# Kernel optimization log

Hardware: AMD Instinct MI355X
Metric: run time of the kernel (lower is better)

The kernel has to match this reference:

```python
import jax, jax.numpy as jnp
import numpy as np

DN = ('NHWC', 'HWIO', 'NHWC')

def _conv1x1(x, k):
    # 1x1 conv, stride 1, SAME padding (channels_last)
    return jax.lax.conv_general_dilated(x, k, window_strides=(1, 1), padding='SAME', dimension_numbers=DN)

def setup_inputs() -> dict:
    key = jax.random.key(0)
    k1, k2, k3, k4, k5 = jax.random.split(key, 5)
    B, H, W, C = 4, 64, 64, 256
    c8 = C // 8
    x = jax.random.normal(k1, (B, H, W, C), dtype=jnp.float32)
    # Glorot-like scaling for stability
    kernel_f = jax.random.normal(k2, (1, 1, C, c8), dtype=jnp.float32) * (1.0 / np.sqrt(C))
    kernel_g = jax.random.normal(k3, (1, 1, C, c8), dtype=jnp.float32) * (1.0 / np.sqrt(C))
    kernel_h = jax.random.normal(k4, (1, 1, C, C), dtype=jnp.float32) * (1.0 / np.sqrt(C))
    gamma = jax.random.normal(k5, (), dtype=jnp.float32) * 0.1
    return {'x': x, 'kernel_f': kernel_f, 'kernel_g': kernel_g, 'kernel_h': kernel_h, 'gamma': gamma}

def reference(x, kernel_f, kernel_g, kernel_h, gamma):
    B, H, W, C = x.shape
    N = H * W
    f = _conv1x1(x, kernel_f).reshape(B, N, -1)   # [B, N, C/8] queries
    g = _conv1x1(x, kernel_g).reshape(B, N, -1)   # [B, N, C/8] keys
    h = _conv1x1(x, kernel_h).reshape(B, N, -1)   # [B, N, C]   values
    e = jnp.einsum('bnc,bmc->bnm', f, g)          # [B, N, N] scores
    attn = jax.nn.softmax(e, axis=-1)
    o = jnp.einsum('bnm,bmc->bnc', attn, h).reshape(B, H, W, C)
    return x + gamma * o
```

## Files before the change

kernel.cpp:

```cpp
#include <hip/hip_runtime.h>

typedef __attribute__((ext_vector_type(8))) short bf16x8;
typedef __attribute__((ext_vector_type(4))) float f32x4;
typedef __attribute__((ext_vector_type(16))) float f32x16;

__device__ __forceinline__ unsigned short f2bf(float f) {
    union { float f; unsigned u; } v; v.f = f;
    return (unsigned short)((v.u + 0x7FFFu + ((v.u >> 16) & 1u)) >> 16);
}
__device__ __forceinline__ unsigned f2bf2_fast(float a, float b) {
    union { float f; unsigned u; } va, vb; va.f = a; vb.f = b;
    return ((va.u + 0x8000u) >> 16) | ((vb.u + 0x8000u) & 0xFFFF0000u);
}

__device__ __forceinline__ void async16(unsigned short* lds, const unsigned short* gsrc) {
    __builtin_amdgcn_global_load_lds(
        (const __attribute__((address_space(1))) void*)gsrc,
        (__attribute__((address_space(3))) void*)lds, 16, 0, 0);
}

__global__ __launch_bounds__(256) void k_wt(const float* __restrict__ kf,
                                            const float* __restrict__ kg,
                                            const float* __restrict__ kh,
                                            unsigned short* __restrict__ wt) {
    int n = blockIdx.x, t = threadIdx.x;
    const float* src; int stride, col;
    if (n < 32)      { src = kf; stride = 32;  col = n; }
    else if (n < 64) { src = kg; stride = 32;  col = n - 32; }
    else             { src = kh; stride = 256; col = n - 64; }
    wt[n * 256 + (((t >> 3) ^ (n & 7)) << 3) + (t & 7)] = f2bf(src[t * stride + col]);
}

__global__ __launch_bounds__(512) void k_proj(const float* __restrict__ x,
                                              const unsigned short* __restrict__ wt,
                                              unsigned short* __restrict__ f,
                                              unsigned short* __restrict__ g,
                                              unsigned short* __restrict__ hT) {
    __shared__ unsigned short xs[16384];
    __shared__ unsigned short ws[2][16384];
    int t = threadIdx.x, rb = blockIdx.x;
    int w = t >> 6, lane = t & 63, q = lane >> 4, n15 = lane & 15;
    int b = rb >> 6, nbase = (rb & 63) * 64;

#pragma unroll
    for (int i = 0; i < 8; ++i) {
        int lin = i * 512 + t, row = lin >> 6, c4 = lin & 63;
        float4 v = *(const float4*)&x[(rb * 64 + row) * 256 + c4 * 4];
        ushort4 o; o.x = f2bf(v.x); o.y = f2bf(v.y); o.z = f2bf(v.z); o.w = f2bf(v.w);
        *(ushort4*)&xs[row * 256 + (((c4 >> 1) ^ (row & 7)) << 3) + ((c4 & 1) << 2)] = o;
    }
#pragma unroll
    for (int j = 0; j < 4; ++j)
        async16(&ws[0][(j * 512 + w * 64) * 8], wt + (j * 512 + t) * 8);

    for (int ct = 0; ct < 5; ++ct) {
        int cur = ct & 1, nxt = cur ^ 1;
        __syncthreads();
        if (ct < 4) {
            const unsigned short* wsrc = wt + (ct + 1) * 16384;
#pragma unroll
            for (int j = 0; j < 4; ++j)
                async16(&ws[nxt][(j * 512 + w * 64) * 8], wsrc + (j * 512 + t) * 8);
        }
        const unsigned short* wcur = ws[cur];
        f32x4 acc[2];
        acc[0] = (f32x4){0.f, 0.f, 0.f, 0.f};
        acc[1] = (f32x4){0.f, 0.f, 0.f, 0.f};

        if (ct == 0) {
            int rg = w & 3, cg = w >> 2;
#pragma unroll
            for (int kk = 0; kk < 8; ++kk) {
                bf16x8 a = *(const bf16x8*)&xs[(rg * 16 + n15) * 256
                                + ((((kk << 2) + q) ^ (n15 & 7)) << 3)];
#pragma unroll
                for (int nt = 0; nt < 2; ++nt) {
                    bf16x8 bw = *(const bf16x8*)&wcur[(cg * 32 + nt * 16 + n15) * 256
                                    + ((((kk << 2) + q) ^ (n15 & 7)) << 3)];
                    acc[nt] = __builtin_amdgcn_mfma_f32_16x16x32_bf16(a, bw, acc[nt], 0, 0, 0);
                }
            }
#pragma unroll
            for (int nt = 0; nt < 2; ++nt)
#pragma unroll
                for (int r = 0; r < 4; ++r) {
                    int grow = rb * 64 + rg * 16 + q * 4 + r;
                    int col = cg * 32 + nt * 16 + n15;
                    unsigned short v = f2bf(acc[nt][r]);
                    if (col < 32) f[grow * 32 + col] = v;
                    else          g[grow * 32 + (col - 32)] = v;
                }
        } else {
            int cg = w & 3, rg = w >> 2;
#pragma unroll
            for (int kk = 0; kk < 8; ++kk) {
                bf16x8 a = *(const bf16x8*)&wcur[(cg * 16 + n15) * 256
                                + ((((kk << 2) + q) ^ (n15 & 7)) << 3)];
#pragma unroll
                for (int nt = 0; nt < 2; ++nt) {
                    bf16x8 bx = *(const bf16x8*)&xs[(rg * 32 + nt * 16 + n15) * 256
                                    + ((((kk << 2) + q) ^ (n15 & 7)) << 3)];
                    acc[nt] = __builtin_amdgcn_mfma_f32_16x16x32_bf16(a, bx, acc[nt], 0, 0, 0);
                }
            }
#pragma unroll
            for (int nt = 0; nt < 2; ++nt)
#pragma unroll
                for (int r = 0; r < 4; ++r) {
                    int ch = (ct - 1) * 64 + cg * 16 + q * 4 + r;
                    int nloc = nbase + rg * 32 + nt * 16 + n15;
                    hT[b * 1048576 + ch * 4096 + nloc] = f2bf(acc[nt][r]);
                }
        }
    }
}

__global__ __launch_bounds__(512, 4) void k_attn(const float* __restrict__ x,
                                                 const unsigned short* __restrict__ f,
                                                 const unsigned short* __restrict__ g,
                                                 const unsigned short* __restrict__ hT,
                                                 const float* __restrict__ gamma_p,
                                                 float* __restrict__ out) {
    __shared__ unsigned short hs[2][8192];
    __shared__ unsigned short pls[2][4096];
    __shared__ float lrec[64];
    int t = threadIdx.x, bx = blockIdx.x;
    int b = (bx >> 1) & 3;
    int ch2 = (bx >> 3) & 1;
    int qt = ((bx & 1) << 5) | (bx >> 4);
    int qbase = qt * 64;
    int chbase = ch2 * 128;
    int w = t >> 6, l = t & 63;
    int hi = l >> 5, l31 = l & 31;
    int q = l >> 4, n15 = l & 15;
    int cb = w & 3;
    const bool is_s = (w < 4);

    bf16x8 aFB;
    if (is_s)
        aFB = *(const bf16x8*)&f[(b * 4096 + qbase + w * 16 + n15) * 32 + q * 8];

    const unsigned short* hsrc = hT + b * 1048576 + (chbase + (t >> 3)) * 4096
                               + (((t & 7) ^ ((t >> 3) & 7)) << 3);

    const unsigned short* gbase = g + (b * 4096 + n15) * 32 + q * 8;
    bf16x8 aG[4], aGn[4];

    f32x16 o0, o1;
#pragma unroll
    for (int i = 0; i < 16; ++i) { o0[i] = 0.f; o1[i] = 0.f; }
    float l_acc = 0.f;
    const f32x4 zero4 = (f32x4){0.f, 0.f, 0.f, 0.f};

    auto s_tile = [&](int buf) {
        f32x4 sa[4];
#pragma unroll
        for (int nt = 0; nt < 4; ++nt)
            sa[nt] = __builtin_amdgcn_mfma_f32_16x16x32_bf16(aG[nt], aFB, zero4, 0, 0, 0);
#pragma unroll
        for (int nt = 0; nt < 4; ++nt)
#pragma unroll
            for (int r = 0; r < 4; ++r) {
                sa[nt][r] = __expf(sa[nt][r]);
                l_acc += sa[nt][r];
            }
#pragma unroll
        for (int nt = 0; nt < 4; ++nt) {
            unsigned p0 = f2bf2_fast(sa[nt][0], sa[nt][1]);
            unsigned p1 = f2bf2_fast(sa[nt][2], sa[nt][3]);
            int kq = 4 * nt + q;
            unsigned* dst = (unsigned*)&pls[buf][(w * 16 + n15) * 64]
                          + ((kq >> 1) ^ (n15 & 7)) * 4 + (kq & 1) * 2;
            dst[0] = p0; dst[1] = p1;
        }
    };

    async16(&hs[0][w * 512], hsrc);
    async16(&hs[0][4096 + w * 512], hsrc + 64 * 4096);
    if (is_s) {
#pragma unroll
        for (int nt = 0; nt < 4; ++nt)
            aG[nt] = *(const bf16x8*)&gbase[(nt * 16) * 32];
#pragma unroll
        for (int nt = 0; nt < 4; ++nt)
            aGn[nt] = *(const bf16x8*)&gbase[(64 + nt * 16) * 32];
        s_tile(0);
#pragma unroll
        for (int nt = 0; nt < 4; ++nt) aG[nt] = aGn[nt];
    }
    __syncthreads();

    for (int kt = 0; kt < 64; ++kt) {
        int cur = kt & 1, nxt = cur ^ 1;

        if (kt + 1 < 64) {
            const unsigned short* hp = hsrc + (kt + 1) * 64;
            async16(&hs[nxt][w * 512], hp);
            async16(&hs[nxt][4096 + w * 512], hp + 64 * 4096);
        }

        if (is_s) {
            if (kt + 1 < 64) {
                int ktn = (kt + 2 < 64) ? kt + 2 : 63;
#pragma unroll
                for (int nt = 0; nt < 4; ++nt)
                    aGn[nt] = *(const bf16x8*)&gbase[(ktn * 64 + nt * 16) * 32];
                s_tile(nxt);
#pragma unroll
                for (int nt = 0; nt < 4; ++nt) aG[nt] = aGn[nt];
            }
        } else {
            const unsigned short* hcur = &hs[cur][0];
            const unsigned short* pcur = &pls[cur][0];
#pragma unroll
            for (int ks = 0; ks < 4; ++ks) {
                int seg = (((2 * ks + hi) ^ (l31 & 7)) << 3);
                bf16x8 bH  = *(const bf16x8*)&hcur[(cb * 32 + l31) * 64 + seg];
                bf16x8 aP0 = *(const bf16x8*)&pcur[l31 * 64 + seg];
                bf16x8 aP1 = *(const bf16x8*)&pcur[(32 + l31) * 64 + seg];
                o0 = __builtin_amdgcn_mfma_f32_32x32x16_bf16(aP0, bH, o0, 0, 0, 0);
                o1 = __builtin_amdgcn_mfma_f32_32x32x16_bf16(aP1, bH, o1, 0, 0, 0);
            }
        }

        __syncthreads();
    }

    if (is_s) {
        float ps = l_acc;
        ps += __shfl_xor(ps, 16);
        ps += __shfl_xor(ps, 32);
        if (q == 0) lrec[w * 16 + n15] = 1.0f / ps;
    }
    __syncthreads();
    if (!is_s) {
        float gam = *gamma_p;
        int ch = chbase + cb * 32 + l31;
#pragma unroll
        for (int qq = 0; qq < 4; ++qq) {
            int r0 = 8 * qq + 4 * hi;
            f32x4 ri0 = *(const f32x4*)&lrec[r0];
            f32x4 ri1 = *(const f32x4*)&lrec[32 + r0];
#pragma unroll
            for (int j = 0; j < 4; ++j) {
                int idx0 = (b * 4096 + qbase + r0 + j) * 256 + ch;
                int idx1 = idx0 + 32 * 256;
                out[idx0] = x[idx0] + gam * (o0[4 * qq + j] * ri0[j]);
                out[idx1] = x[idx1] + gam * (o1[4 * qq + j] * ri1[j]);
            }
        }
    }
}

extern "C" void kernel_launch(void* const* d_in, const int* in_sizes, int n_in,
                              void* d_out, int out_size, void* d_ws, size_t ws_size,
                              hipStream_t stream) {
    const float* x  = (const float*)d_in[0];
    const float* kf = (const float*)d_in[1];
    const float* kg = (const float*)d_in[2];
    const float* kh = (const float*)d_in[3];
    const float* gm = (const float*)d_in[4];
    float* out = (float*)d_out;

    char* ws = (char*)d_ws;
    unsigned short* wt = (unsigned short*)(ws);
    unsigned short* fb = (unsigned short*)(ws + 163840);
    unsigned short* gb = (unsigned short*)(ws + 1212416);
    unsigned short* hT = (unsigned short*)(ws + 2260992);

    hipLaunchKernelGGL(k_wt,   dim3(320), dim3(256), 0, stream, kf, kg, kh, wt);
    hipLaunchKernelGGL(k_proj, dim3(256), dim3(512), 0, stream, x, wt, fb, gb, hT);
    hipLaunchKernelGGL(k_attn, dim3(512), dim3(512), 0, stream, x, fb, gb, hT, gm, out);
}
```

Measured before the change: 150.8 us.

## Restructure attention block to cover all channels with 12 waves and direct V loads

Each attention block now handles all 256 output channels with 768 threads (4 score waves plus 8 PV waves), halving the grid and removing the duplicated score/exp computation that the two channel-half blocks previously each did. Score waves are re-split by key columns instead of query rows, with per-wave partial row sums reduced through shared memory. V tiles are loaded straight from global memory into registers with double buffering instead of async copies into LDS. The log2(e) factor is folded into the query weights so exp2 can replace expf. The trade-off is higher register pressure, per-lane global loads of V, and fewer blocks in flight.

```diff
diff --git a/kernel.cpp b/kernel.cpp
--- a/kernel.cpp
+++ b/kernel.cpp
@@ -11,6 +11,14 @@
 __device__ __forceinline__ unsigned f2bf2_fast(float a, float b) {
     union { float f; unsigned u; } va, vb; va.f = a; vb.f = b;
     return ((va.u + 0x8000u) >> 16) | ((vb.u + 0x8000u) & 0xFFFF0000u);
+}
+
+__device__ __forceinline__ float fexp2(float v) {
+#if __has_builtin(__builtin_amdgcn_exp2f)
+    return __builtin_amdgcn_exp2f(v);
+#else
+    float r; asm("v_exp_f32 %0, %1" : "=v"(r) : "v"(v)); return r;
+#endif
 }
 
 __device__ __forceinline__ void async16(unsigned short* lds, const unsigned short* gsrc) {
@@ -28,7 +36,9 @@
     if (n < 32)      { src = kf; stride = 32;  col = n; }
     else if (n < 64) { src = kg; stride = 32;  col = n - 32; }
     else             { src = kh; stride = 256; col = n - 64; }
-    wt[n * 256 + (((t >> 3) ^ (n & 7)) << 3) + (t & 7)] = f2bf(src[t * stride + col]);
+    float v = src[t * stride + col];
+    if (n < 32) v *= 1.44269504088896341f;
+    wt[n * 256 + (((t >> 3) ^ (n & 7)) << 3) + (t & 7)] = f2bf(v);
 }
 
 __global__ __launch_bounds__(512) void k_proj(const float* __restrict__ x,
@@ -115,127 +125,126 @@
     }
 }
 
-__global__ __launch_bounds__(512, 4) void k_attn(const float* __restrict__ x,
+__global__ __launch_bounds__(768, 3) void k_attn(const float* __restrict__ x,
                                                  const unsigned short* __restrict__ f,
                                                  const unsigned short* __restrict__ g,
                                                  const unsigned short* __restrict__ hT,
                                                  const float* __restrict__ gamma_p,
                                                  float* __restrict__ out) {
-    __shared__ unsigned short hs[2][8192];
     __shared__ unsigned short pls[2][4096];
-    __shared__ float lrec[64];
+    __shared__ float lpart[4][64];
+    __shared__ __align__(16) float lrec[64];
     int t = threadIdx.x, bx = blockIdx.x;
     int b = (bx >> 1) & 3;
-    int ch2 = (bx >> 3) & 1;
-    int qt = ((bx & 1) << 5) | (bx >> 4);
+    int qt = ((bx & 1) << 5) | (bx >> 3);
     int qbase = qt * 64;
-    int chbase = ch2 * 128;
     int w = t >> 6, l = t & 63;
     int hi = l >> 5, l31 = l & 31;
     int q = l >> 4, n15 = l & 15;
-    int cb = w & 3;
+    int cb = w - 4;
     const bool is_s = (w < 4);
 
-    bf16x8 aFB;
-    if (is_s)
-        aFB = *(const bf16x8*)&f[(b * 4096 + qbase + w * 16 + n15) * 32 + q * 8];
-
-    const unsigned short* hsrc = hT + b * 1048576 + (chbase + (t >> 3)) * 4096
-                               + (((t & 7) ^ ((t >> 3) & 7)) << 3);
-
-    const unsigned short* gbase = g + (b * 4096 + n15) * 32 + q * 8;
-    bf16x8 aG[4], aGn[4];
-
-    f32x16 o0, o1;
-#pragma unroll
-    for (int i = 0; i < 16; ++i) { o0[i] = 0.f; o1[i] = 0.f; }
-    float l_acc = 0.f;
+    bf16x8 aFB[4];
+    const unsigned short* gW = g + (b * 4096 + w * 16 + n15) * 32 + q * 8;
+    if (is_s) {
+#pragma unroll
+        for (int nt = 0; nt < 4; ++nt)
+            aFB[nt] = *(const bf16x8*)&f[(b * 4096 + qbase + nt * 16 + n15) * 32 + q * 8];
+    }
+    bf16x8 aG, aGn;
+    f32x4 lac = (f32x4){0.f, 0.f, 0.f, 0.f};
     const f32x4 zero4 = (f32x4){0.f, 0.f, 0.f, 0.f};
 
     auto s_tile = [&](int buf) {
         f32x4 sa[4];
 #pragma unroll
         for (int nt = 0; nt < 4; ++nt)
-            sa[nt] = __builtin_amdgcn_mfma_f32_16x16x32_bf16(aG[nt], aFB, zero4, 0, 0, 0);
-#pragma unroll
-        for (int nt = 0; nt < 4; ++nt)
+            sa[nt] = __builtin_amdgcn_mfma_f32_16x16x32_bf16(aG, aFB[nt], zero4, 0, 0, 0);
+        int kq = w * 4 + q;
+#pragma unroll
+        for (int nt = 0; nt < 4; ++nt) {
 #pragma unroll
             for (int r = 0; r < 4; ++r) {
-                sa[nt][r] = __expf(sa[nt][r]);
-                l_acc += sa[nt][r];
-            }
-#pragma unroll
-        for (int nt = 0; nt < 4; ++nt) {
+                sa[nt][r] = fexp2(sa[nt][r]);
+                lac[nt] += sa[nt][r];
+            }
             unsigned p0 = f2bf2_fast(sa[nt][0], sa[nt][1]);
             unsigned p1 = f2bf2_fast(sa[nt][2], sa[nt][3]);
-            int kq = 4 * nt + q;
-            unsigned* dst = (unsigned*)&pls[buf][(w * 16 + n15) * 64]
-                          + ((kq >> 1) ^ (n15 & 7)) * 4 + (kq & 1) * 2;
+            int row = nt * 16 + n15;
+            unsigned* dst = (unsigned*)&pls[buf][row * 64]
+                          + (((kq >> 1) ^ (n15 & 7)) << 2) + ((kq & 1) << 1);
             dst[0] = p0; dst[1] = p1;
         }
     };
 
-    async16(&hs[0][w * 512], hsrc);
-    async16(&hs[0][4096 + w * 512], hsrc + 64 * 4096);
+    const unsigned short* hrow = hT + b * 1048576 + (cb * 32 + l31) * 4096 + hi * 8;
+    f32x16 o0, o1;
+#pragma unroll
+    for (int i = 0; i < 16; ++i) { o0[i] = 0.f; o1[i] = 0.f; }
+    bf16x8 bHc[4], bHn[4];
+
     if (is_s) {
-#pragma unroll
-        for (int nt = 0; nt < 4; ++nt)
-            aG[nt] = *(const bf16x8*)&gbase[(nt * 16) * 32];
-#pragma unroll
-        for (int nt = 0; nt < 4; ++nt)
-            aGn[nt] = *(const bf16x8*)&gbase[(64 + nt * 16) * 32];
+        aG  = *(const bf16x8*)&gW[0];
+        aGn = *(const bf16x8*)&gW[2048];
         s_tile(0);
-#pragma unroll
-        for (int nt = 0; nt < 4; ++nt) aG[nt] = aGn[nt];
+        aG = aGn;
+    } else {
+#pragma unroll
+        for (int ks = 0; ks < 4; ++ks)
+            bHc[ks] = *(const bf16x8*)&hrow[ks * 16];
     }
     __syncthreads();
 
+#pragma unroll 2
     for (int kt = 0; kt < 64; ++kt) {
         int cur = kt & 1, nxt = cur ^ 1;
-
-        if (kt + 1 < 64) {
-            const unsigned short* hp = hsrc + (kt + 1) * 64;
-            async16(&hs[nxt][w * 512], hp);
-            async16(&hs[nxt][4096 + w * 512], hp + 64 * 4096);
-        }
 
         if (is_s) {
             if (kt + 1 < 64) {
                 int ktn = (kt + 2 < 64) ? kt + 2 : 63;
-#pragma unroll
-                for (int nt = 0; nt < 4; ++nt)
-                    aGn[nt] = *(const bf16x8*)&gbase[(ktn * 64 + nt * 16) * 32];
+                aGn = *(const bf16x8*)&gW[ktn * 2048];
                 s_tile(nxt);
-#pragma unroll
-                for (int nt = 0; nt < 4; ++nt) aG[nt] = aGn[nt];
+                aG = aGn;
             }
         } else {
-            const unsigned short* hcur = &hs[cur][0];
+            if (kt + 1 < 64) {
+                const unsigned short* hp = hrow + (kt + 1) * 64;
+#pragma unroll
+                for (int ks = 0; ks < 4; ++ks)
+                    bHn[ks] = *(const bf16x8*)&hp[ks * 16];
+            }
             const unsigned short* pcur = &pls[cur][0];
 #pragma unroll
             for (int ks = 0; ks < 4; ++ks) {
                 int seg = (((2 * ks + hi) ^ (l31 & 7)) << 3);
-                bf16x8 bH  = *(const bf16x8*)&hcur[(cb * 32 + l31) * 64 + seg];
                 bf16x8 aP0 = *(const bf16x8*)&pcur[l31 * 64 + seg];
                 bf16x8 aP1 = *(const bf16x8*)&pcur[(32 + l31) * 64 + seg];
-                o0 = __builtin_amdgcn_mfma_f32_32x32x16_bf16(aP0, bH, o0, 0, 0, 0);
-                o1 = __builtin_amdgcn_mfma_f32_32x32x16_bf16(aP1, bH, o1, 0, 0, 0);
-            }
-        }
-
+                o0 = __builtin_amdgcn_mfma_f32_32x32x16_bf16(aP0, bHc[ks], o0, 0, 0, 0);
+                o1 = __builtin_amdgcn_mfma_f32_32x32x16_bf16(aP1, bHc[ks], o1, 0, 0, 0);
+            }
+            if (kt + 1 < 64) {
+#pragma unroll
+                for (int ks = 0; ks < 4; ++ks) bHc[ks] = bHn[ks];
+            }
+        }
         __syncthreads();
     }
 
     if (is_s) {
-        float ps = l_acc;
-        ps += __shfl_xor(ps, 16);
-        ps += __shfl_xor(ps, 32);
-        if (q == 0) lrec[w * 16 + n15] = 1.0f / ps;
-    }
+#pragma unroll
+        for (int nt = 0; nt < 4; ++nt) {
+            float ps = lac[nt];
+            ps += __shfl_xor(ps, 16);
+            ps += __shfl_xor(ps, 32);
+            if (q == 0) lpart[w][nt * 16 + n15] = ps;
+        }
+    }
+    __syncthreads();
+    if (t < 64) lrec[t] = 1.0f / (lpart[0][t] + lpart[1][t] + lpart[2][t] + lpart[3][t]);
     __syncthreads();
     if (!is_s) {
         float gam = *gamma_p;
-        int ch = chbase + cb * 32 + l31;
+        int ch = cb * 32 + l31;
 #pragma unroll
         for (int qq = 0; qq < 4; ++qq) {
             int r0 = 8 * qq + 4 * hi;
@@ -270,5 +279,5 @@
 
     hipLaunchKernelGGL(k_wt,   dim3(320), dim3(256), 0, stream, kf, kg, kh, wt);
     hipLaunchKernelGGL(k_proj, dim3(256), dim3(512), 0, stream, x, wt, fb, gb, hT);
-    hipLaunchKernelGGL(k_attn, dim3(512), dim3(512), 0, stream, x, fb, gb, hT, gm, out);
-}
+    hipLaunchKernelGGL(k_attn, dim3(256), dim3(768), 0, stream, x, fb, gb, hT, gm, out);
+}
```

Result: slower. 178.6 us (+18.4%).
